# Optimization experiments

Hardware: AMD Instinct MI355X
Metric: run time of the kernel (lower is better)

The kernel has to match this reference:

```python
import jax, jax.numpy as jnp
import numpy as np

K = 121          # kernel_size
C = 3            # channels
PAD = (K - 1) // 2  # 60, replicate padding so output matches input spatial size


def setup_inputs() -> dict:
    key = jax.random.key(0)
    k1, k2 = jax.random.split(key)
    x = jax.random.normal(k1, (8, C, 512, 512), dtype=jnp.float32)
    sigma = jax.random.uniform(k2, (), dtype=jnp.float32)
    return {"x": x, "sigma": sigma}


def _gaussian_kernel(sigma):
    # sigma -> sigma*8 + 16, variance = sigma**2 (as in torch forward)
    s = sigma * 8.0 + 16.0
    variance = s * s
    coord = jnp.arange(K, dtype=jnp.float32) - (K - 1) / 2.0  # centered coords
    diff = -(coord[:, None] ** 2 + coord[None, :] ** 2)       # [K,K], -((x-m)^2+(y-m)^2)
    kern = jnp.exp(diff / (2.0 * variance))
    # the 1/(2*pi*variance) prefactor cancels under normalization
    kern = kern / jnp.sum(kern)
    return kern


def reference(x, sigma):
    kern = _gaussian_kernel(sigma)
    # depthwise weights: [out_ch=C, in_ch/groups=1, K, K]
    w = jnp.broadcast_to(kern[None, None, :, :], (C, 1, K, K))
    # replicate padding (torch 'replicate' == jnp 'edge')
    xp = jnp.pad(x, ((0, 0), (0, 0), (PAD, PAD), (PAD, PAD)), mode="edge")
    out = jax.lax.conv_general_dilated(
        xp, w,
        window_strides=(1, 1),
        padding="VALID",
        dimension_numbers=("NCHW", "OIHW", "NCHW"),
        feature_group_count=C,
    )
    return out
```

## Files before the change

kernel.cpp:

```cpp
#include <hip/hip_runtime.h>


#define HH    512
#define WW    512
#define PLANE (512 * 512)
#define NIMG  24
#define ROWF  672

__global__ void wk_prep(const float* __restrict__ sigma,
                        float* __restrict__ wg) {
    const int tid = threadIdx.x;
    const float s = sigma[0] * 8.0f + 16.0f;
    const float inv2v = 1.0f / (2.0f * s * s);
    float sum = 0.0f;
    #pragma unroll
    for (int k = 0; k <= 120; ++k) {
        const float c = (float)k - 60.0f;
        sum += __expf(-c * c * inv2v);
    }
    float g = 0.0f;
    if (tid < 121) {
        const float c = (float)tid - 60.0f;
        g = __expf(-c * c * inv2v);
    }
    wg[tid] = g / sum;
}

__device__ __forceinline__ int swz_off(int col) {
    const int u = col >> 2;
    return ((u ^ ((u >> 3) & 7)) << 2) + (col & 3);
}

#define V_OCT_P(A, B, C, KO)                                              \
    { _Pragma("unroll")                                                   \
      for (int ki = 0; ki < 8; ++ki) {                                    \
          int rr = r0 - 44 + (KO) * 8 + ki;                               \
          rr = rr < 0 ? 0 : (rr > HH - 1 ? HH - 1 : rr);                  \
          C[ki] = *(const float2*)&src[(size_t)rr * WW];                  \
      }                                                                   \
      *(float4*)&wq[0] = *(const float4*)&wg[(KO) * 8];                   \
      *(float4*)&wq[4] = *(const float4*)&wg[(KO) * 8 + 4];               \
      _Pragma("unroll")                                                   \
      for (int ki = 0; ki < 8; ++ki) {                                    \
          const float wk = wq[ki];                                        \
          _Pragma("unroll")                                               \
          for (int j = 0; j < 8; ++j) {                                   \
              const int idx = ki + j;                                     \
              const float2 v = (idx < 8) ? A[idx] : B[idx - 8];           \
              vac[j].x += wk * v.x; vac[j].y += wk * v.y;                 \
          }                                                               \
      }                                                                   \
    }

#define V_OCT_NP(A, B, KO)                                                \
    { *(float4*)&wq[0] = *(const float4*)&wg[(KO) * 8];                   \
      *(float4*)&wq[4] = *(const float4*)&wg[(KO) * 8 + 4];               \
      _Pragma("unroll")                                                   \
      for (int ki = 0; ki < 8; ++ki) {                                    \
          const float wk = wq[ki];                                        \
          _Pragma("unroll")                                               \
          for (int j = 0; j < 8; ++j) {                                   \
              const int idx = ki + j;                                     \
              const float2 v = (idx < 8) ? A[idx] : B[idx - 8];           \
              vac[j].x += wk * v.x; vac[j].y += wk * v.y;                 \
          }                                                               \
      }                                                                   \
    }

#define LOADG2(DA, DB, G)                                                 \
    { const int u_  = 2 * (G);                                            \
      const int o1_ = (u_ ^ ((u_ >> 3) & 7)) << 2;                        \
      const int o2_ = o1_ ^ 4;                                            \
      *(float4*)&DA[0] = *(const float4*)(bs + o1_);                      \
      *(float4*)&DA[4] = *(const float4*)(bs + o2_);                      \
      *(float4*)&DB[0] = *(const float4*)(bs + o1_ + 256);                \
      *(float4*)&DB[4] = *(const float4*)(bs + o2_ + 256); }

#define H_OCT2(A0, A1, A2, A3, B0, B1, B2, B3, KO)                        \
    { LOADG2(A3, B3, L + (KO) + 3)                                        \
      *(float4*)&wq[0] = *(const float4*)&wg[(KO) * 8];                   \
      *(float4*)&wq[4] = *(const float4*)&wg[(KO) * 8 + 4];               \
      _Pragma("unroll")                                                   \
      for (int ki = 0; ki < 8; ++ki) {                                    \
          const float wk = wq[ki];                                        \
          _Pragma("unroll")                                               \
          for (int j = 0; j < 8; ++j) {                                   \
              const int idx = ki + j;                                     \
              const float vA = (idx < 8) ? A0[idx]                        \
                             : (idx < 16) ? A1[idx - 8] : A2[idx - 16];   \
              const float vB = (idx < 8) ? B0[idx]                        \
                             : (idx < 16) ? B1[idx - 8] : B2[idx - 16];   \
              accA[j] += wk * vA;                                         \
              accB[j] += wk * vB;                                         \
          }                                                               \
      }                                                                   \
    }

__global__ __launch_bounds__(256, 6) void blur_fused(
        const float* __restrict__ x, const float* __restrict__ wg,
        float* __restrict__ out) {
    __shared__ float sm[8 * ROWF];
    const int tid = threadIdx.x;

    const int lid   = blockIdx.x + gridDim.x * blockIdx.y;
    const int tile  = (lid & 7) * 192 + (lid >> 3);
    const int r0    = (tile & 63) * 8;
    const int plane = tile >> 6;

    const int c0 = tid * 2;
    const float* __restrict__ src = x + (size_t)plane * PLANE + c0;

    float2 w0[8], w1[8], w2[8], vac[8];
    float  wq[8];
    #pragma unroll
    for (int m = 0; m < 8; ++m) {
        int rr = r0 - 60 + m;
        rr = rr < 0 ? 0 : rr;
        w0[m] = *(const float2*)&src[(size_t)rr * WW];
    }
    #pragma unroll
    for (int m = 0; m < 8; ++m) {
        int rr = r0 - 52 + m;
        rr = rr < 0 ? 0 : rr;
        w1[m] = *(const float2*)&src[(size_t)rr * WW];
    }
    #pragma unroll
    for (int j = 0; j < 8; ++j) vac[j] = make_float2(0.f, 0.f);

    #pragma unroll 1
    for (int ko = 0; ko < 15; ko += 3) {
        V_OCT_P(w0, w1, w2, ko)
        V_OCT_P(w1, w2, w0, ko + 1)
        V_OCT_P(w2, w0, w1, ko + 2)
    }
    V_OCT_NP(w0, w1, 15)

    {
        const int off = swz_off(c0 + 60);
        #pragma unroll
        for (int j = 0; j < 8; ++j)
            *(float2*)&sm[j * ROWF + off] = vac[j];
    }
    __syncthreads();

    if (tid < 36) {
        const int p = (tid < 15) ? tid * 4
                    : (tid < 34) ? 572 + (tid - 15) * 4
                                 : 648 + (tid - 34) * 4;
        const int u   = p >> 2;
        const int off = (u ^ ((u >> 3) & 7)) << 2;
        const int soff = (tid < 15) ? swz_off(60) : swz_off(571);
        #pragma unroll
        for (int r8 = 0; r8 < 8; ++r8) {
            const float v = (tid < 34) ? sm[r8 * ROWF + soff] : 0.0f;
            *(float4*)&sm[r8 * ROWF + off] = make_float4(v, v, v, v);
        }
    }
    __syncthreads();

    const int r = tid >> 5;
    const int L = tid & 31;
    const float* __restrict__ bs = sm + r * ROWF;

    float a0[8], a1[8], a2[8], a3[8];
    float b0[8], b1[8], b2[8], b3[8];
    float accA[8], accB[8];
    #pragma unroll
    for (int j = 0; j < 8; ++j) { accA[j] = 0.0f; accB[j] = 0.0f; }

    LOADG2(a0, b0, L)
    LOADG2(a1, b1, L + 1)
    LOADG2(a2, b2, L + 2)

    #pragma unroll 1
    for (int ko = 0; ko < 16; ko += 4) {
        H_OCT2(a0, a1, a2, a3, b0, b1, b2, b3, ko)
        H_OCT2(a1, a2, a3, a0, b1, b2, b3, b0, ko + 1)
        H_OCT2(a2, a3, a0, a1, b2, b3, b0, b1, ko + 2)
        H_OCT2(a3, a0, a1, a2, b3, b0, b1, b2, ko + 3)
    }

    float* __restrict__ dst = out + (size_t)plane * PLANE
                                  + (size_t)(r0 + r) * WW + L * 8;
    *(float4*)(dst)       = make_float4(accA[0], accA[1], accA[2], accA[3]);
    *(float4*)(dst + 4)   = make_float4(accA[4], accA[5], accA[6], accA[7]);
    *(float4*)(dst + 256) = make_float4(accB[0], accB[1], accB[2], accB[3]);
    *(float4*)(dst + 260) = make_float4(accB[4], accB[5], accB[6], accB[7]);
}

extern "C" void kernel_launch(void* const* d_in, const int* in_sizes, int n_in,
                              void* d_out, int out_size, void* d_ws, size_t ws_size,
                              hipStream_t stream) {
    const float* x     = (const float*)d_in[0];
    const float* sigma = (const float*)d_in[1];
    float* out = (float*)d_out;
    float* wg  = (float*)d_ws;
    wk_prep<<<dim3(1), dim3(128), 0, stream>>>(sigma, wg);
    blur_fused<<<dim3(HH / 8, NIMG), dim3(256), 0, stream>>>(x, wg, out);
}
```

Baseline: 113.9 us.

## Compute 16 contiguous outputs per thread in horizontal pass with shuffle-based store remap

The horizontal convolution now has each thread produce 16 contiguous outputs from a single sliding register window, instead of two separate 8-output windows 256 columns apart. This halves the LDS reads per output and removes the duplicated window registers. Outputs are exchanged between lanes 16 apart with an xor shuffle so the global stores keep their previous coalesced layout. The cost is the extra shuffles and a changed LDS access pattern, since adjacent lanes now read groups 2L, which may introduce bank conflicts under the existing swizzle.

```diff
diff --git a/kernel.cpp b/kernel.cpp
--- a/kernel.cpp
+++ b/kernel.cpp
@@ -67,31 +67,41 @@
       }                                                                   \
     }
 
-#define LOADG2(DA, DB, G)                                                 \
+#define LOADG(D, G)                                                       \
     { const int u_  = 2 * (G);                                            \
       const int o1_ = (u_ ^ ((u_ >> 3) & 7)) << 2;                        \
-      const int o2_ = o1_ ^ 4;                                            \
-      *(float4*)&DA[0] = *(const float4*)(bs + o1_);                      \
-      *(float4*)&DA[4] = *(const float4*)(bs + o2_);                      \
-      *(float4*)&DB[0] = *(const float4*)(bs + o1_ + 256);                \
-      *(float4*)&DB[4] = *(const float4*)(bs + o2_ + 256); }
-
-#define H_OCT2(A0, A1, A2, A3, B0, B1, B2, B3, KO)                        \
-    { LOADG2(A3, B3, L + (KO) + 3)                                        \
+      *(float4*)&D[0] = *(const float4*)(bs + o1_);                       \
+      *(float4*)&D[4] = *(const float4*)(bs + (o1_ ^ 4)); }
+
+#define H_OCT16(A0, A1, A2, A3, KO)                                       \
+    { LOADG(A3, 2 * L + (KO) + 3)                                         \
       *(float4*)&wq[0] = *(const float4*)&wg[(KO) * 8];                   \
       *(float4*)&wq[4] = *(const float4*)&wg[(KO) * 8 + 4];               \
       _Pragma("unroll")                                                   \
       for (int ki = 0; ki < 8; ++ki) {                                    \
           const float wk = wq[ki];                                        \
           _Pragma("unroll")                                               \
-          for (int j = 0; j < 8; ++j) {                                   \
-              const int idx = ki + j;                                     \
-              const float vA = (idx < 8) ? A0[idx]                        \
-                             : (idx < 16) ? A1[idx - 8] : A2[idx - 16];   \
-              const float vB = (idx < 8) ? B0[idx]                        \
-                             : (idx < 16) ? B1[idx - 8] : B2[idx - 16];   \
-              accA[j] += wk * vA;                                         \
-              accB[j] += wk * vB;                                         \
+          for (int j = 0; j < 16; ++j) {                                  \
+              const int idx = ki + j;                                     \
+              const float v = (idx < 8) ? A0[idx]                         \
+                            : (idx < 16) ? A1[idx - 8] : A2[idx - 16];    \
+              acc[j] += wk * v;                                           \
+          }                                                               \
+      }                                                                   \
+    }
+
+#define H_OCT16_NP(A0, A1, A2, A3, KO)                                    \
+    { *(float4*)&wq[0] = *(const float4*)&wg[(KO) * 8];                   \
+      *(float4*)&wq[4] = *(const float4*)&wg[(KO) * 8 + 4];               \
+      _Pragma("unroll")                                                   \
+      for (int ki = 0; ki < 8; ++ki) {                                    \
+          const float wk = wq[ki];                                        \
+          _Pragma("unroll")                                               \
+          for (int j = 0; j < 16; ++j) {                                  \
+              const int idx = ki + j;                                     \
+              const float v = (idx < 8) ? A0[idx]                         \
+                            : (idx < 16) ? A1[idx - 8] : A2[idx - 16];    \
+              acc[j] += wk * v;                                           \
           }                                                               \
       }                                                                   \
     }
@@ -163,29 +173,44 @@
     const float* __restrict__ bs = sm + r * ROWF;
 
     float a0[8], a1[8], a2[8], a3[8];
-    float b0[8], b1[8], b2[8], b3[8];
-    float accA[8], accB[8];
-    #pragma unroll
-    for (int j = 0; j < 8; ++j) { accA[j] = 0.0f; accB[j] = 0.0f; }
-
-    LOADG2(a0, b0, L)
-    LOADG2(a1, b1, L + 1)
-    LOADG2(a2, b2, L + 2)
+    float acc[16];
+    #pragma unroll
+    for (int j = 0; j < 16; ++j) acc[j] = 0.0f;
+
+    LOADG(a0, 2 * L)
+    LOADG(a1, 2 * L + 1)
+    LOADG(a2, 2 * L + 2)
 
     #pragma unroll 1
-    for (int ko = 0; ko < 16; ko += 4) {
-        H_OCT2(a0, a1, a2, a3, b0, b1, b2, b3, ko)
-        H_OCT2(a1, a2, a3, a0, b1, b2, b3, b0, ko + 1)
-        H_OCT2(a2, a3, a0, a1, b2, b3, b0, b1, ko + 2)
-        H_OCT2(a3, a0, a1, a2, b3, b0, b1, b2, ko + 3)
-    }
-
-    float* __restrict__ dst = out + (size_t)plane * PLANE
-                                  + (size_t)(r0 + r) * WW + L * 8;
-    *(float4*)(dst)       = make_float4(accA[0], accA[1], accA[2], accA[3]);
-    *(float4*)(dst + 4)   = make_float4(accA[4], accA[5], accA[6], accA[7]);
-    *(float4*)(dst + 256) = make_float4(accB[0], accB[1], accB[2], accB[3]);
-    *(float4*)(dst + 260) = make_float4(accB[4], accB[5], accB[6], accB[7]);
+    for (int ko = 0; ko < 12; ko += 4) {
+        H_OCT16(a0, a1, a2, a3, ko)
+        H_OCT16(a1, a2, a3, a0, ko + 1)
+        H_OCT16(a2, a3, a0, a1, ko + 2)
+        H_OCT16(a3, a0, a1, a2, ko + 3)
+    }
+    H_OCT16   (a0, a1, a2, a3, 12)
+    H_OCT16   (a1, a2, a3, a0, 13)
+    H_OCT16   (a2, a3, a0, a1, 14)
+    H_OCT16_NP(a3, a0, a1, a2, 15)
+
+    {
+        const int sel = (L >> 4) & 1;
+        float blk1[8], blk2[8];
+        #pragma unroll
+        for (int j = 0; j < 8; ++j) {
+            const float send = sel ? acc[j] : acc[j + 8];
+            const float recv = __shfl_xor(send, 16, 64);
+            blk1[j] = sel ? recv : acc[j];
+            blk2[j] = sel ? acc[j + 8] : recv;
+        }
+        float* __restrict__ dst = out + (size_t)plane * PLANE
+                                      + (size_t)(r0 + r) * WW
+                                      + 16 * (L & 15) + sel * 8;
+        *(float4*)(dst)       = make_float4(blk1[0], blk1[1], blk1[2], blk1[3]);
+        *(float4*)(dst + 4)   = make_float4(blk1[4], blk1[5], blk1[6], blk1[7]);
+        *(float4*)(dst + 256) = make_float4(blk2[0], blk2[1], blk2[2], blk2[3]);
+        *(float4*)(dst + 260) = make_float4(blk2[4], blk2[5], blk2[6], blk2[7]);
+    }
 }
 
 extern "C" void kernel_launch(void* const* d_in, const int* in_sizes, int n_in,
```

Result: slower. 126.5 us (+11.0%).
